# Kernel tuning notes

Measured on AMD Instinct MI355X. Metric: run time of the kernel, lower is better.

Reference implementation:

```python
import jax, jax.numpy as jnp
import numpy as np

N_HEADS = 16
D_HEAD = 128
D_MODEL = N_HEADS * D_HEAD  # 2048


def setup_inputs() -> dict:
    key = jax.random.key(0)
    k1, k2, k3 = jax.random.split(key, 3)
    B, S = 2, 2048
    x = jax.random.normal(k1, (B, S, D_MODEL), dtype=jnp.float32)
    W_qkv = jax.random.normal(k2, (D_MODEL, 3 * D_MODEL), dtype=jnp.float32) / np.sqrt(D_MODEL)
    b_qkv = jnp.zeros((3 * D_MODEL,), dtype=jnp.float32)
    W_out = jax.random.normal(k3, (D_MODEL, D_MODEL), dtype=jnp.float32) / np.sqrt(D_MODEL)
    b_out = jnp.zeros((D_MODEL,), dtype=jnp.float32)
    return {"x": x, "W_qkv": W_qkv, "b_qkv": b_qkv, "W_out": W_out, "b_out": b_out}


def reference(x, W_qkv, b_qkv, W_out, b_out):
    B, S, _ = x.shape
    qkv = x @ W_qkv + b_qkv                      # [B, S, 3*d_model]
    q, k, v = jnp.split(qkv, 3, axis=-1)
    # [B, S, d_model] -> [B, n_heads, S, d_head]
    reshape = lambda t: t.reshape(B, S, N_HEADS, D_HEAD).transpose(0, 2, 1, 3)
    q, k, v = reshape(q), reshape(k), reshape(v)
    scale = 1.0 / jnp.sqrt(jnp.asarray(D_HEAD, dtype=x.dtype))
    attn = jnp.einsum('bhqd,bhkd->bhqk', q, k) * scale  # [B, H, S, S]
    causal = jnp.arange(S)[:, None] >= jnp.arange(S)[None, :]
    masked = jnp.where(causal, attn, jnp.asarray(-jnp.inf, dtype=attn.dtype))
    probs = jax.nn.softmax(masked, axis=-1)
    out = jnp.einsum('bhqk,bhkd->bhqd', probs, v)       # [B, H, S, d_head]
    out = out.transpose(0, 2, 1, 3).reshape(B, S, D_MODEL)
    return out @ W_out + b_out
```

## Files before the change

### kernel.cpp

```cpp
#include <hip/hip_runtime.h>
#include <stdint.h>

#define BATCH 2
#define SEQ   2048
#define NH    16
#define DH    128
#define DM    2048
#define NQKV  6144
#define MROWS 4096

typedef __bf16 bf16x8 __attribute__((ext_vector_type(8)));
typedef float  f32x4  __attribute__((ext_vector_type(4)));

#define FENCE() __asm__ __volatile__("" ::: "memory")

__device__ __forceinline__ void gl_lds16(const void* g, void* l) {
  __builtin_amdgcn_global_load_lds(
      (const __attribute__((address_space(1))) void*)g,
      (__attribute__((address_space(3))) void*)l, 16, 0, 0);
}

__device__ __forceinline__ unsigned short f2bf(float f) {
  uint32_t u = __builtin_bit_cast(uint32_t, f);
  return (unsigned short)((u + 0x7FFFu + ((u >> 16) & 1u)) >> 16);
}

template <int N>
__device__ __forceinline__ float dpp_ror(float x) {
  int r = __builtin_amdgcn_update_dpp(__builtin_bit_cast(int, x),
                                      __builtin_bit_cast(int, x),
                                      0x120 | N, 0xF, 0xF, false);
  return __builtin_bit_cast(float, r);
}
__device__ __forceinline__ float red16_max(float x) {
  x = fmaxf(x, dpp_ror<1>(x)); x = fmaxf(x, dpp_ror<2>(x));
  x = fmaxf(x, dpp_ror<4>(x)); x = fmaxf(x, dpp_ror<8>(x));
  return x;
}
__device__ __forceinline__ float red16_sum(float x) {
  x += dpp_ror<1>(x); x += dpp_ror<2>(x);
  x += dpp_ror<4>(x); x += dpp_ror<8>(x);
  return x;
}

__global__ void convert_x_kernel(const float* __restrict__ in,
                                 unsigned short* __restrict__ out) {
  int i = blockIdx.x * 256 + threadIdx.x;
  float4 v = ((const float4*)in)[i];
  uint32_t lo = (uint32_t)f2bf(v.x) | ((uint32_t)f2bf(v.y) << 16);
  uint32_t hi = (uint32_t)f2bf(v.z) | ((uint32_t)f2bf(v.w) << 16);
  ((uint2*)out)[i] = make_uint2(lo, hi);
}

__global__ void transpose_w_kernel(const float* __restrict__ in,
                                   unsigned short* __restrict__ out,
                                   int K, int N) {
  __shared__ float tile[32][33];
  const int tx = threadIdx.x, ty = threadIdx.y;
  const int n0 = blockIdx.x * 32, k0 = blockIdx.y * 32;
  #pragma unroll
  for (int i = 0; i < 32; i += 8)
    tile[ty + i][tx] = in[(size_t)(k0 + ty + i) * N + n0 + tx];
  __syncthreads();
  #pragma unroll
  for (int i = 0; i < 32; i += 8)
    out[(size_t)(n0 + ty + i) * K + k0 + tx] = f2bf(tile[tx][ty + i]);
}

__global__ void qkv_gemm_kernel(const unsigned short* __restrict__ A,
                                const unsigned short* __restrict__ Bt,
                                const float* __restrict__ bias,
                                unsigned short* __restrict__ Qb,
                                unsigned short* __restrict__ Kb,
                                unsigned short* __restrict__ Vtb) {
  __shared__ alignas(16) unsigned short As[128 * 32];
  __shared__ alignas(16) unsigned short Bs[128 * 32];
  const int tid = threadIdx.x;
  const int lane = tid & 63, wave = tid >> 6;
  const int wm = wave >> 1, wn = wave & 1;
  const int quad = lane >> 4, l15 = lane & 15;
  const int bm = blockIdx.x, bn = blockIdx.y;
  const int K = DM;

  f32x4 acc[4][4];
  #pragma unroll
  for (int i = 0; i < 4; ++i)
    #pragma unroll
    for (int j = 0; j < 4; ++j) acc[i][j] = (f32x4){0.f, 0.f, 0.f, 0.f};

  const unsigned short* Ag = A + (size_t)(bm * 128 + (tid >> 2)) * K + (tid & 3) * 8;
  const unsigned short* Bg = Bt + (size_t)(bn * 128 + (tid >> 2)) * K + (tid & 3) * 8;

  for (int kt = 0; kt < K / 32; ++kt) {
    gl_lds16(Ag + kt * 32,                  As + tid * 8);
    gl_lds16(Ag + (size_t)64 * K + kt * 32, As + 2048 + tid * 8);
    gl_lds16(Bg + kt * 32,                  Bs + tid * 8);
    gl_lds16(Bg + (size_t)64 * K + kt * 32, Bs + 2048 + tid * 8);
    __syncthreads();
    bf16x8 af[4], bfr[4];
    #pragma unroll
    for (int mi = 0; mi < 4; ++mi)
      af[mi] = *(const bf16x8*)(As + (wm * 64 + mi * 16 + l15) * 32 + quad * 8);
    #pragma unroll
    for (int ni = 0; ni < 4; ++ni)
      bfr[ni] = *(const bf16x8*)(Bs + (wn * 64 + ni * 16 + l15) * 32 + quad * 8);
    #pragma unroll
    for (int mi = 0; mi < 4; ++mi)
      #pragma unroll
      for (int ni = 0; ni < 4; ++ni)
        acc[mi][ni] = __builtin_amdgcn_mfma_f32_16x16x32_bf16(af[mi], bfr[ni], acc[mi][ni], 0, 0, 0);
    __syncthreads();
  }

  #pragma unroll
  for (int mi = 0; mi < 4; ++mi) {
    #pragma unroll
    for (int ni = 0; ni < 4; ++ni) {
      const int grow0 = bm * 128 + wm * 64 + mi * 16 + quad * 4;
      const int gcol  = bn * 128 + wn * 64 + ni * 16 + l15;
      const float bv = bias[gcol];
      const int which = gcol >> 11;
      const int rem = gcol & 2047;
      const int h = rem >> 7, d = rem & 127;
      #pragma unroll
      for (int r = 0; r < 4; ++r) {
        const int grow = grow0 + r;
        const int b = grow >> 11, s = grow & 2047;
        const int bh = b * NH + h;
        const unsigned short val = f2bf(acc[mi][ni][r] + bv);
        if (which == 0)      Qb[((size_t)bh * SEQ + s) * DH + d] = val;
        else if (which == 1) Kb[((size_t)bh * SEQ + s) * DH + d] = val;
        else
          Vtb[(((size_t)bh * 32 + (s >> 6)) * 128 + d) * 64 + (s & 63)] = val;
      }
    }
  }
}

#define PS_LD 72
__global__ __launch_bounds__(256, 2)
void attn_kernel(const unsigned short* __restrict__ Qb,
                 const unsigned short* __restrict__ Kb,
                 const unsigned short* __restrict__ Vtb,
                 unsigned short* __restrict__ Ob) {
  __shared__ alignas(16) unsigned short lds_all[33792];
  unsigned short* Ks  = lds_all;
  unsigned short* Vs0 = lds_all + 8192;
  unsigned short* Vs1 = lds_all + 16384;
  const int tid = threadIdx.x, lane = tid & 63, wave = tid >> 6;
  unsigned short* Ps = lds_all + 24576 + wave * (32 * PS_LD);
  const int quad = lane >> 4, l15 = lane & 15;
  const int bh = blockIdx.y;
  const int b = bh >> 4, h = bh & 15;
  const float c = 0.08838834764831845f * 1.4426950408889634f;

  const unsigned short* Kbase = Kb + (size_t)bh * SEQ * DH;
  const unsigned short* Vbase = Vtb + (size_t)bh * 32 * 8192;

  for (int half = 0; half < 2; ++half) {
    const int qb = half ? (int)blockIdx.x : 15 - (int)blockIdx.x;
    const int q0 = qb * 128 + wave * 32;

    __syncthreads();

    auto stage_k = [&](int kt) {
      const unsigned short* kg = Kbase + (size_t)kt * 64 * DH;
      #pragma unroll
      for (int r = 0; r < 4; ++r) {
        const int idx = r * 256 + tid;
        const int krow = idx >> 4, kchunk = (idx & 15) ^ (krow & 7);
        gl_lds16(kg + krow * DH + kchunk * 8, Ks + idx * 8);
      }
    };
    auto stage_v = [&](int kt, unsigned short* vs) {
      const unsigned short* vg = Vbase + (size_t)kt * 8192;
      #pragma unroll
      for (int r = 0; r < 4; ++r) {
        const int idx = r * 256 + tid;
        const int vrow = idx >> 3, vchunk = (idx & 7) ^ (vrow & 7);
        gl_lds16(vg + vrow * 64 + vchunk * 8, vs + idx * 8);
      }
    };

    bf16x8 qf[2][4];
    #pragma unroll
    for (int mi = 0; mi < 2; ++mi)
      #pragma unroll
      for (int ds = 0; ds < 4; ++ds)
        qf[mi][ds] = *(const bf16x8*)(Qb + ((size_t)bh * SEQ + q0 + mi * 16 + l15) * DH + ds * 32 + quad * 8);

    f32x4 o[2][8];
    #pragma unroll
    for (int mi = 0; mi < 2; ++mi)
      #pragma unroll
      for (int di = 0; di < 8; ++di) o[mi][di] = (f32x4){0.f, 0.f, 0.f, 0.f};
    float m_i[2][4], l_i[2][4];
    #pragma unroll
    for (int mi = 0; mi < 2; ++mi)
      #pragma unroll
      for (int r = 0; r < 4; ++r) { m_i[mi][r] = -INFINITY; l_i[mi][r] = 0.f; }

    const int nkt = (qb + 1) * 2;

    stage_v(0, Vs0);
    stage_k(0);
    __builtin_amdgcn_s_waitcnt(0x0F70);
    FENCE(); __builtin_amdgcn_s_barrier(); FENCE();

    for (int kt = 0; kt < nkt; ++kt) {
      unsigned short* Vcur = (kt & 1) ? Vs1 : Vs0;
      const bool more = (kt + 1 < nkt);
      if (more) stage_v(kt + 1, (kt & 1) ? Vs0 : Vs1);
      FENCE();

      f32x4 s_acc[2][4];
      #pragma unroll
      for (int mi = 0; mi < 2; ++mi)
        #pragma unroll
        for (int ni = 0; ni < 4; ++ni) s_acc[mi][ni] = (f32x4){0.f, 0.f, 0.f, 0.f};
      #pragma unroll
      for (int ds = 0; ds < 4; ++ds) {
        bf16x8 kf[4];
        #pragma unroll
        for (int ni = 0; ni < 4; ++ni) {
          const int krow = ni * 16 + l15;
          const int kc = (ds * 4 + quad) ^ (krow & 7);
          kf[ni] = *(const bf16x8*)(Ks + (krow * 16 + kc) * 8);
        }
        #pragma unroll
        for (int mi = 0; mi < 2; ++mi)
          #pragma unroll
          for (int ni = 0; ni < 4; ++ni)
            s_acc[mi][ni] = __builtin_amdgcn_mfma_f32_16x16x32_bf16(qf[mi][ds], kf[ni], s_acc[mi][ni], 0, 0, 0);
      }

      FENCE(); __builtin_amdgcn_s_barrier(); FENCE();
      if (more) stage_k(kt + 1);
      FENCE();

      if (kt * 64 + 63 > q0) {
        #pragma unroll
        for (int mi = 0; mi < 2; ++mi)
          #pragma unroll
          for (int ni = 0; ni < 4; ++ni) {
            const int kcol = kt * 64 + ni * 16 + l15;
            #pragma unroll
            for (int r = 0; r < 4; ++r) {
              float v = s_acc[mi][ni][r] * c;
              const int qrow = q0 + mi * 16 + quad * 4 + r;
              if (kcol > qrow) v = -INFINITY;
              s_acc[mi][ni][r] = v;
            }
          }
      } else {
        #pragma unroll
        for (int mi = 0; mi < 2; ++mi)
          #pragma unroll
          for (int ni = 0; ni < 4; ++ni)
            #pragma unroll
            for (int r = 0; r < 4; ++r) s_acc[mi][ni][r] *= c;
      }

      #pragma unroll
      for (int mi = 0; mi < 2; ++mi) {
        float rmax[4], alpha[4], rsum[4];
        #pragma unroll
        for (int r = 0; r < 4; ++r) {
          float m0 = fmaxf(fmaxf(s_acc[mi][0][r], s_acc[mi][1][r]),
                           fmaxf(s_acc[mi][2][r], s_acc[mi][3][r]));
          rmax[r] = red16_max(m0);
        }
        #pragma unroll
        for (int r = 0; r < 4; ++r) {
          const float mnew = fmaxf(m_i[mi][r], rmax[r]);
          alpha[r] = exp2f(m_i[mi][r] - mnew);
          m_i[mi][r] = mnew;
        }
        #pragma unroll
        for (int r = 0; r < 4; ++r) {
          float s0 = 0.f;
          #pragma unroll
          for (int ni = 0; ni < 4; ++ni) {
            const float p = exp2f(s_acc[mi][ni][r] - m_i[mi][r]);
            s_acc[mi][ni][r] = p;
            s0 += p;
          }
          rsum[r] = red16_sum(s0);
        }
        #pragma unroll
        for (int r = 0; r < 4; ++r) l_i[mi][r] = l_i[mi][r] * alpha[r] + rsum[r];
        #pragma unroll
        for (int di = 0; di < 8; ++di)
          #pragma unroll
          for (int r = 0; r < 4; ++r) o[mi][di][r] *= alpha[r];
        #pragma unroll
        for (int ni = 0; ni < 4; ++ni)
          #pragma unroll
          for (int r = 0; r < 4; ++r)
            Ps[(mi * 16 + quad * 4 + r) * PS_LD + ni * 16 + l15] = f2bf(s_acc[mi][ni][r]);
      }
      FENCE();

      #pragma unroll
      for (int ks = 0; ks < 2; ++ks) {
        bf16x8 pf[2];
        #pragma unroll
        for (int mi = 0; mi < 2; ++mi)
          pf[mi] = *(const bf16x8*)(Ps + (mi * 16 + l15) * PS_LD + ks * 32 + quad * 8);
        #pragma unroll
        for (int di = 0; di < 8; ++di) {
          const int vrow = di * 16 + l15;
          const int vc = (ks * 4 + quad) ^ (vrow & 7);
          const bf16x8 vf = *(const bf16x8*)(Vcur + (vrow * 8 + vc) * 8);
          #pragma unroll
          for (int mi = 0; mi < 2; ++mi)
            o[mi][di] = __builtin_amdgcn_mfma_f32_16x16x32_bf16(pf[mi], vf, o[mi][di], 0, 0, 0);
        }
      }

      if (more) {
        __builtin_amdgcn_s_waitcnt(0x0F70);
        FENCE(); __builtin_amdgcn_s_barrier(); FENCE();
      }
    }

    __syncthreads();
    {
      unsigned short* Osc = lds_all + wave * (32 * 136);
      #pragma unroll
      for (int mi = 0; mi < 2; ++mi) {
        float inv[4];
        #pragma unroll
        for (int r = 0; r < 4; ++r) inv[r] = 1.0f / l_i[mi][r];
        #pragma unroll
        for (int di = 0; di < 8; ++di)
          #pragma unroll
          for (int r = 0; r < 4; ++r)
            Osc[(mi * 16 + quad * 4 + r) * 136 + di * 16 + l15] = f2bf(o[mi][di][r] * inv[r]);
      }
      __syncthreads();
      FENCE();
      #pragma unroll
      for (int rh = 0; rh < 2; ++rh)
        #pragma unroll
        for (int cg = 0; cg < 4; ++cg) {
          const int row = rh * 16 + (lane >> 2);
          const bf16x8 v8 = *(const bf16x8*)(Osc + row * 136 + cg * 32 + (lane & 3) * 8);
          *(bf16x8*)(Ob + ((size_t)(b * SEQ + q0 - wave * 32 + wave * 32 + row)) * DM + h * DH + cg * 32 + (lane & 3) * 8) = v8;
        }
    }
  }
}

__global__ void out_gemm_kernel(const unsigned short* __restrict__ A,
                                const unsigned short* __restrict__ Bt,
                                const float* __restrict__ bias,
                                float* __restrict__ out) {
  __shared__ alignas(16) unsigned short As[128 * 32];
  __shared__ alignas(16) unsigned short Bs[128 * 32];
  const int tid = threadIdx.x;
  const int lane = tid & 63, wave = tid >> 6;
  const int wm = wave >> 1, wn = wave & 1;
  const int quad = lane >> 4, l15 = lane & 15;
  const int bm = blockIdx.x, bn = blockIdx.y;
  const int K = DM;

  f32x4 acc[4][4];
  #pragma unroll
  for (int i = 0; i < 4; ++i)
    #pragma unroll
    for (int j = 0; j < 4; ++j) acc[i][j] = (f32x4){0.f, 0.f, 0.f, 0.f};

  const unsigned short* Ag = A + (size_t)(bm * 128 + (tid >> 2)) * K + (tid & 3) * 8;
  const unsigned short* Bg = Bt + (size_t)(bn * 128 + (tid >> 2)) * K + (tid & 3) * 8;

  for (int kt = 0; kt < K / 32; ++kt) {
    gl_lds16(Ag + kt * 32,                  As + tid * 8);
    gl_lds16(Ag + (size_t)64 * K + kt * 32, As + 2048 + tid * 8);
    gl_lds16(Bg + kt * 32,                  Bs + tid * 8);
    gl_lds16(Bg + (size_t)64 * K + kt * 32, Bs + 2048 + tid * 8);
    __syncthreads();
    bf16x8 af[4], bfr[4];
    #pragma unroll
    for (int mi = 0; mi < 4; ++mi)
      af[mi] = *(const bf16x8*)(As + (wm * 64 + mi * 16 + l15) * 32 + quad * 8);
    #pragma unroll
    for (int ni = 0; ni < 4; ++ni)
      bfr[ni] = *(const bf16x8*)(Bs + (wn * 64 + ni * 16 + l15) * 32 + quad * 8);
    #pragma unroll
    for (int mi = 0; mi < 4; ++mi)
      #pragma unroll
      for (int ni = 0; ni < 4; ++ni)
        acc[mi][ni] = __builtin_amdgcn_mfma_f32_16x16x32_bf16(af[mi], bfr[ni], acc[mi][ni], 0, 0, 0);
    __syncthreads();
  }

  #pragma unroll
  for (int mi = 0; mi < 4; ++mi) {
    #pragma unroll
    for (int ni = 0; ni < 4; ++ni) {
      const int grow0 = bm * 128 + wm * 64 + mi * 16 + quad * 4;
      const int gcol  = bn * 128 + wn * 64 + ni * 16 + l15;
      const float bv = bias[gcol];
      #pragma unroll
      for (int r = 0; r < 4; ++r)
        out[(size_t)(grow0 + r) * DM + gcol] = acc[mi][ni][r] + bv;
    }
  }
}

extern "C" void kernel_launch(void* const* d_in, const int* in_sizes, int n_in,
                              void* d_out, int out_size, void* d_ws, size_t ws_size,
                              hipStream_t stream) {
  const float* x     = (const float*)d_in[0];
  const float* W_qkv = (const float*)d_in[1];
  const float* b_qkv = (const float*)d_in[2];
  const float* W_out = (const float*)d_in[3];
  const float* b_out = (const float*)d_in[4];
  float* out = (float*)d_out;

  char* ws = (char*)d_ws;
  unsigned short* xb    = (unsigned short*)(ws);
  unsigned short* WqkvT = (unsigned short*)(ws + 16777216ull);
  unsigned short* WoutT = (unsigned short*)(ws + 41943040ull);
  unsigned short* Qb    = (unsigned short*)(ws + 50331648ull);
  unsigned short* Kb    = (unsigned short*)(ws + 67108864ull);
  unsigned short* Vtb   = (unsigned short*)(ws + 83886080ull);
  unsigned short* attnb = (unsigned short*)(ws + 100663296ull);

  convert_x_kernel<<<dim3(8192), dim3(256), 0, stream>>>(x, xb);
  transpose_w_kernel<<<dim3(192, 64), dim3(32, 8), 0, stream>>>(W_qkv, WqkvT, DM, NQKV);
  transpose_w_kernel<<<dim3(64, 64), dim3(32, 8), 0, stream>>>(W_out, WoutT, DM, DM);
  qkv_gemm_kernel<<<dim3(32, 48), dim3(256), 0, stream>>>(xb, WqkvT, b_qkv, Qb, Kb, Vtb);
  attn_kernel<<<dim3(8, 32), dim3(256), 0, stream>>>(Qb, Kb, Vtb, attnb);
  out_gemm_kernel<<<dim3(32, 16), dim3(256), 0, stream>>>(attnb, WoutT, b_out, out);
}
```

Before: 436.8 us.

## Merge prep kernels and deepen QKV GEMM K-tile with XOR-swizzled LDS

The three preprocessing launches (x conversion and two weight transposes) become a single launch that dispatches on block index. The QKV GEMM K-step grows from 32 to 64, halving the number of barrier pairs per output tile, and the LDS tile layout is XOR-swizzled to avoid bank conflicts on fragment reads. A redundant index expression in the attention store is also simplified. LDS use per block doubles, which may lower occupancy.

After: 425.9 us. 2.5% less time.

```diff
diff --git a/kernel.cpp b/kernel.cpp
--- a/kernel.cpp
+++ b/kernel.cpp
@@ -43,21 +43,27 @@
   return x;
 }
 
-__global__ void convert_x_kernel(const float* __restrict__ in,
-                                 unsigned short* __restrict__ out) {
-  int i = blockIdx.x * 256 + threadIdx.x;
-  float4 v = ((const float4*)in)[i];
-  uint32_t lo = (uint32_t)f2bf(v.x) | ((uint32_t)f2bf(v.y) << 16);
-  uint32_t hi = (uint32_t)f2bf(v.z) | ((uint32_t)f2bf(v.w) << 16);
-  ((uint2*)out)[i] = make_uint2(lo, hi);
-}
-
-__global__ void transpose_w_kernel(const float* __restrict__ in,
-                                   unsigned short* __restrict__ out,
-                                   int K, int N) {
+__global__ void prep_kernel(const float* __restrict__ x,
+                            const float* __restrict__ W_qkv,
+                            const float* __restrict__ W_out,
+                            unsigned short* __restrict__ xb,
+                            unsigned short* __restrict__ WqkvT,
+                            unsigned short* __restrict__ WoutT) {
   __shared__ float tile[32][33];
-  const int tx = threadIdx.x, ty = threadIdx.y;
-  const int n0 = blockIdx.x * 32, k0 = blockIdx.y * 32;
+  const int bid = blockIdx.x, tid = threadIdx.x;
+  if (bid < 8192) {
+    const int i = bid * 256 + tid;
+    float4 v = ((const float4*)x)[i];
+    uint32_t lo = (uint32_t)f2bf(v.x) | ((uint32_t)f2bf(v.y) << 16);
+    uint32_t hi = (uint32_t)f2bf(v.z) | ((uint32_t)f2bf(v.w) << 16);
+    ((uint2*)xb)[i] = make_uint2(lo, hi);
+    return;
+  }
+  const float* in; unsigned short* out; int K, N, bx, by;
+  if (bid < 20480) { const int rel = bid - 8192;  in = W_qkv; out = WqkvT; K = DM; N = NQKV; bx = rel % 192; by = rel / 192; }
+  else             { const int rel = bid - 20480; in = W_out; out = WoutT; K = DM; N = DM;   bx = rel % 64;  by = rel / 64; }
+  const int tx = tid & 31, ty = tid >> 5;
+  const int n0 = bx * 32, k0 = by * 32;
   #pragma unroll
   for (int i = 0; i < 32; i += 8)
     tile[ty + i][tx] = in[(size_t)(k0 + ty + i) * N + n0 + tx];
@@ -73,8 +79,8 @@
                                 unsigned short* __restrict__ Qb,
                                 unsigned short* __restrict__ Kb,
                                 unsigned short* __restrict__ Vtb) {
-  __shared__ alignas(16) unsigned short As[128 * 32];
-  __shared__ alignas(16) unsigned short Bs[128 * 32];
+  __shared__ alignas(16) unsigned short As[128 * 64];
+  __shared__ alignas(16) unsigned short Bs[128 * 64];
   const int tid = threadIdx.x;
   const int lane = tid & 63, wave = tid >> 6;
   const int wm = wave >> 1, wn = wave & 1;
@@ -88,27 +94,36 @@
     #pragma unroll
     for (int j = 0; j < 4; ++j) acc[i][j] = (f32x4){0.f, 0.f, 0.f, 0.f};
 
-  const unsigned short* Ag = A + (size_t)(bm * 128 + (tid >> 2)) * K + (tid & 3) * 8;
-  const unsigned short* Bg = Bt + (size_t)(bn * 128 + (tid >> 2)) * K + (tid & 3) * 8;
-
-  for (int kt = 0; kt < K / 32; ++kt) {
-    gl_lds16(Ag + kt * 32,                  As + tid * 8);
-    gl_lds16(Ag + (size_t)64 * K + kt * 32, As + 2048 + tid * 8);
-    gl_lds16(Bg + kt * 32,                  Bs + tid * 8);
-    gl_lds16(Bg + (size_t)64 * K + kt * 32, Bs + 2048 + tid * 8);
-    __syncthreads();
-    bf16x8 af[4], bfr[4];
-    #pragma unroll
-    for (int mi = 0; mi < 4; ++mi)
-      af[mi] = *(const bf16x8*)(As + (wm * 64 + mi * 16 + l15) * 32 + quad * 8);
-    #pragma unroll
-    for (int ni = 0; ni < 4; ++ni)
-      bfr[ni] = *(const bf16x8*)(Bs + (wn * 64 + ni * 16 + l15) * 32 + quad * 8);
-    #pragma unroll
-    for (int mi = 0; mi < 4; ++mi)
-      #pragma unroll
-      for (int ni = 0; ni < 4; ++ni)
-        acc[mi][ni] = __builtin_amdgcn_mfma_f32_16x16x32_bf16(af[mi], bfr[ni], acc[mi][ni], 0, 0, 0);
+  for (int kt = 0; kt < K / 64; ++kt) {
+    #pragma unroll
+    for (int r = 0; r < 4; ++r) {
+      const int idx = r * 256 + tid;
+      const int row = idx >> 3, chunk = (idx & 7) ^ (row & 7);
+      gl_lds16(A  + (size_t)(bm * 128 + row) * K + kt * 64 + chunk * 8, As + idx * 8);
+      gl_lds16(Bt + (size_t)(bn * 128 + row) * K + kt * 64 + chunk * 8, Bs + idx * 8);
+    }
+    __syncthreads();
+    #pragma unroll
+    for (int ds = 0; ds < 2; ++ds) {
+      bf16x8 af[4], bfr[4];
+      #pragma unroll
+      for (int mi = 0; mi < 4; ++mi) {
+        const int row = wm * 64 + mi * 16 + l15;
+        const int c = (ds * 4 + quad) ^ (row & 7);
+        af[mi] = *(const bf16x8*)(As + (row * 8 + c) * 8);
+      }
+      #pragma unroll
+      for (int ni = 0; ni < 4; ++ni) {
+        const int row = wn * 64 + ni * 16 + l15;
+        const int c = (ds * 4 + quad) ^ (row & 7);
+        bfr[ni] = *(const bf16x8*)(Bs + (row * 8 + c) * 8);
+      }
+      #pragma unroll
+      for (int mi = 0; mi < 4; ++mi)
+        #pragma unroll
+        for (int ni = 0; ni < 4; ++ni)
+          acc[mi][ni] = __builtin_amdgcn_mfma_f32_16x16x32_bf16(af[mi], bfr[ni], acc[mi][ni], 0, 0, 0);
+    }
     __syncthreads();
   }
 
@@ -346,7 +361,7 @@
         for (int cg = 0; cg < 4; ++cg) {
           const int row = rh * 16 + (lane >> 2);
           const bf16x8 v8 = *(const bf16x8*)(Osc + row * 136 + cg * 32 + (lane & 3) * 8);
-          *(bf16x8*)(Ob + ((size_t)(b * SEQ + q0 - wave * 32 + wave * 32 + row)) * DM + h * DH + cg * 32 + (lane & 3) * 8) = v8;
+          *(bf16x8*)(Ob + ((size_t)(b * SEQ + q0 + row)) * DM + h * DH + cg * 32 + (lane & 3) * 8) = v8;
         }
     }
   }
@@ -428,9 +443,7 @@
   unsigned short* Vtb   = (unsigned short*)(ws + 83886080ull);
   unsigned short* attnb = (unsigned short*)(ws + 100663296ull);
 
-  convert_x_kernel<<<dim3(8192), dim3(256), 0, stream>>>(x, xb);
-  transpose_w_kernel<<<dim3(192, 64), dim3(32, 8), 0, stream>>>(W_qkv, WqkvT, DM, NQKV);
-  transpose_w_kernel<<<dim3(64, 64), dim3(32, 8), 0, stream>>>(W_out, WoutT, DM, DM);
+  prep_kernel<<<dim3(24576), dim3(256), 0, stream>>>(x, W_qkv, W_out, xb, WqkvT, WoutT);
   qkv_gemm_kernel<<<dim3(32, 48), dim3(256), 0, stream>>>(xb, WqkvT, b_qkv, Qb, Kb, Vtb);
   attn_kernel<<<dim3(8, 32), dim3(256), 0, stream>>>(Qb, Kb, Vtb, attnb);
   out_gemm_kernel<<<dim3(32, 16), dim3(256), 0, stream>>>(attnb, WoutT, b_out, out);
```
